# Kernel optimization log

Hardware: AMD Instinct MI355X
Metric: run time of the kernel (lower is better)

The kernel has to match this reference:

```python
import jax, jax.numpy as jnp
import numpy as np

B, C, H, W = 2, 256, 128, 128
L, NH, NP = 4, 8, 4
D = C // NH
HW = H * W


def _pos_emb_2d(h, w, c):
    # positional_encodings.PositionalEncoding2D for channels-last input (B, h, w, c)
    ch = int(np.ceil(c / 4) * 2)
    inv_freq = 1.0 / (10000.0 ** (np.arange(0, ch, 2, dtype=np.float32) / ch))

    def emb(n):
        s = np.arange(n, dtype=np.float32)[:, None] * inv_freq[None, :]
        return np.stack([np.sin(s), np.cos(s)], -1).reshape(n, -1)  # interleaved sin/cos

    out = np.zeros((h, w, 2 * ch), np.float32)
    out[:, :, :ch] = emb(h)[:, None, :]
    out[:, :, ch:2 * ch] = emb(w)[None, :, :]
    return jnp.asarray(out[:, :, :c])


def _offset_bias():
    # init_weights grid_init bias of sampling_offsets
    thetas = np.arange(NH, dtype=np.float32) * (2.0 * np.pi / NH)
    g = np.stack([np.cos(thetas), np.sin(thetas)], -1)
    g = g / np.abs(g).max(-1, keepdims=True)
    g = np.tile(g[:, None, None, :], (1, 1, NP, 1))
    for i in range(NP):
        g[:, :, i, :] *= i + 1
    return np.tile(g.reshape(-1)[None], (L, 1)).astype(np.float32)


def _ref_points(h, w):
    # get_reference_points with scale_ratio == 1 (ratio of equal lidar ranges)
    ry, rx = jnp.meshgrid(jnp.linspace(0.5, h - 0.5, h) / h,
                          jnp.linspace(0.5, w - 0.5, w) / w, indexing='ij')
    return jnp.stack([rx.reshape(-1), ry.reshape(-1)], -1)  # (HW, 2) as (x, y)


def _deform_attn(value, loc, aw, h, w):
    # value: (B,HW,NH,D); loc in [0,1]: (B,HW,NH,NP,2); aw: (B,HW,NH,NP)
    # Matches F.grid_sample(mode='bilinear', padding_mode='zeros', align_corners=False)
    b, q, nh, d = value.shape
    p = loc.shape[3]
    v = value.transpose(0, 2, 1, 3)  # (B, NH, HW, D)
    gx = 2.0 * loc[..., 0] - 1.0
    gy = 2.0 * loc[..., 1] - 1.0
    ix = ((gx + 1.0) * w - 1.0) * 0.5
    iy = ((gy + 1.0) * h - 1.0) * 0.5
    x0 = jnp.floor(ix)
    y0 = jnp.floor(iy)

    def gather(xf, yf):
        valid = (xf >= 0) & (xf <= w - 1) & (yf >= 0) & (yf <= h - 1)
        xi = jnp.clip(xf, 0, w - 1).astype(jnp.int32)
        yi = jnp.clip(yf, 0, h - 1).astype(jnp.int32)
        idx = (yi * w + xi).transpose(0, 2, 1, 3).reshape(b, nh, q * p)
        g = jnp.take_along_axis(v, idx[..., None], axis=2).reshape(b, nh, q, p, d)
        return g * valid.transpose(0, 2, 1, 3)[..., None]

    wx1 = (ix - x0).transpose(0, 2, 1, 3)[..., None]
    wy1 = (iy - y0).transpose(0, 2, 1, 3)[..., None]
    wx0 = 1.0 - wx1
    wy0 = 1.0 - wy1
    s = (gather(x0, y0) * (wx0 * wy0) + gather(x0 + 1.0, y0) * (wx1 * wy0)
         + gather(x0, y0 + 1.0) * (wx0 * wy1) + gather(x0 + 1.0, y0 + 1.0) * (wx1 * wy1))
    out = jnp.einsum('bhqpd,bqhp->bqhd', s, aw)
    return out.reshape(b, q, nh * d)


def setup_inputs() -> dict:
    key = jax.random.key(0)
    ks = jax.random.split(key, 8)
    sc = 1.0 / np.sqrt(C).astype(np.float32)
    return {
        "ego_feature": jax.random.normal(ks[0], (B, C, H, W), jnp.float32),
        "conv_w": jax.random.normal(ks[1], (C, C), jnp.float32) * sc,  # 1x1 conv, (in,out)
        "conv_b": jnp.zeros((C,), jnp.float32),
        "in_scale": jnp.ones((1,), jnp.float32) / 30.0,
        "out_scale": jnp.ones((1,), jnp.float32) / 30.0,
        "off_w": jax.random.normal(ks[2], (L, C, NH * NP * 2), jnp.float32) * 0.01,
        "off_b": jnp.asarray(_offset_bias()),
        "aw_w": jax.random.normal(ks[3], (L, C, NH * NP), jnp.float32) * 0.02,
        "aw_b": jnp.zeros((L, NH * NP), jnp.float32),
        "vp_w": jax.random.normal(ks[4], (L, C, C), jnp.float32) * sc,
        "vp_b": jnp.zeros((L, C), jnp.float32),
        "op_w": jax.random.normal(ks[5], (L, C, C), jnp.float32) * sc,
        "op_b": jnp.zeros((L, C), jnp.float32),
    }


def reference(ego_feature, conv_w, conv_b, in_scale, out_scale, off_w, off_b,
              aw_w, aw_b, vp_w, vp_b, op_w, op_b):
    # PositionalEncodingPermute2D: channels-last PE, permuted to (C,H,W)
    pe_in = _pos_emb_2d(H, W, C).transpose(2, 0, 1)[None]  # (1,C,H,W)
    x = ego_feature + in_scale[0] * pe_in
    key_tok = x.reshape(B, C, HW).transpose(0, 2, 1)  # (B, HW, C)
    # Upsample(scale=1) is identity; 1x1 conv == per-token matmul
    out = key_tok @ conv_w + conv_b
    pe_out = _pos_emb_2d(H, W, C)[None]  # (1,H,W,C)
    ref = _ref_points(H, W)
    norm = jnp.asarray([W, H], jnp.float32)
    for l in range(L):
        o = out.reshape(B, H, W, C) + out_scale[0] * pe_out
        q = o.reshape(B, HW, C)
        identity = q
        v = (key_tok @ vp_w[l] + vp_b[l]).reshape(B, HW, NH, D)
        offs = (q @ off_w[l] + off_b[l]).reshape(B, HW, NH, NP, 2)
        aw = jax.nn.softmax((q @ aw_w[l] + aw_b[l]).reshape(B, HW, NH, NP), axis=-1)
        loc = ref[None, :, None, None, :] + offs / norm
        attn = _deform_attn(v, loc, aw, H, W)
        out = attn @ op_w[l] + op_b[l] + identity  # dropout is identity in eval
    return out  # (B, HW, C)
```

## Files before the change

### kernel.cpp

```cpp
#include <hip/hip_runtime.h>
#include <math.h>

#define HH 128
#define WW 128
#define CCH 256
#define NHH 8
#define NPP 4
#define DDIM 32
#define HWW (HH * WW)
#define BB 2
#define MM (BB * HWW)
#define KK 256

typedef __attribute__((ext_vector_type(8))) __bf16 bf16x8;
typedef __attribute__((ext_vector_type(8))) short s16x8;
typedef __attribute__((ext_vector_type(4))) short s16x4;
typedef __attribute__((ext_vector_type(4))) float f32x4;

#define PE_LOG2_STEP 0.20762050593f

__device__ __forceinline__ float pe_val(int c, int y, int x) {
    int j = (c & 127) >> 1;
    float pos = (c < 128) ? (float)y : (float)x;
    float f = exp2f(-(float)j * PE_LOG2_STEP);
    float s, cs;
    __sincosf(pos * f, &s, &cs);
    return (c & 1) ? cs : s;
}

__device__ __forceinline__ short f2b(float f) {
    union { float f; unsigned u; } c; c.f = f;
    unsigned r = c.u + 0x7FFF + ((c.u >> 16) & 1);
    return (short)(r >> 16);
}

__device__ __forceinline__ float b2f(short s) {
    union { unsigned u; float f; } c;
    c.u = ((unsigned)(unsigned short)s) << 16;
    return c.f;
}

__device__ __forceinline__ void gload16(const short* g, short* l) {
    __builtin_amdgcn_global_load_lds(
        (const __attribute__((address_space(1))) unsigned int*)g,
        (__attribute__((address_space(3))) unsigned int*)l, 16, 0, 0);
}

__global__ __launch_bounds__(256) void pe_table_kernel(
    const float* __restrict__ out_scale, short* __restrict__ pe_b)
{
    int t = blockIdx.x * 256 + threadIdx.x;
    int cp = t & 127;
    int p = t >> 7;
    int y = p >> 7, x = p & 127;
    int c2 = cp * 2;
    int j = (c2 & 127) >> 1;
    float pos = (c2 < 128) ? (float)y : (float)x;
    float f = exp2f(-(float)j * PE_LOG2_STEP);
    float s, c;
    __sincosf(pos * f, &s, &c);
    float sc = out_scale[0];
    pe_b[(size_t)p * CCH + c2] = f2b(sc * s);
    pe_b[(size_t)p * CCH + c2 + 1] = f2b(sc * c);
}

__global__ __launch_bounds__(256) void convert_big_w(
    const float* __restrict__ conv_w, const float* __restrict__ vp_w,
    const float* __restrict__ op_w, short* __restrict__ wt)
{
    __shared__ float tile[32][33];
    int z = blockIdx.z;
    const float* src = (z == 0) ? conv_w
                     : (z <= 4) ? vp_w + (size_t)(z - 1) * KK * CCH
                                : op_w + (size_t)(z - 5) * KK * CCH;
    short* dst = wt + (size_t)z * KK * CCH;
    int k0 = blockIdx.x * 32, n0 = blockIdx.y * 32;
    int tx = threadIdx.x, ty = threadIdx.y;
    #pragma unroll
    for (int i = 0; i < 4; ++i)
        tile[ty + i * 8][tx] = src[(size_t)(k0 + ty + i * 8) * CCH + n0 + tx];
    __syncthreads();
    int t = ty * 32 + tx;
    int n_l = t >> 3, ks = (t & 7) * 4;
    s16x4 o;
    #pragma unroll
    for (int j = 0; j < 4; ++j) o[j] = f2b(tile[ks + j][n_l]);
    *(s16x4*)&dst[(size_t)(n0 + n_l) * KK + k0 + ks] = o;
}

__global__ __launch_bounds__(256) void convert_offaw_w(
    const float* __restrict__ off_w, const float* __restrict__ aw_w,
    const float* __restrict__ off_b, const float* __restrict__ aw_b,
    short* __restrict__ wt, float* __restrict__ bias_cat)
{
    __shared__ float tile[32][33];
    int l = blockIdx.z;
    int nt = blockIdx.y;
    int k0 = blockIdx.x * 32;
    const float* src; int N, ncol0;
    if (nt < 2) { src = off_w + (size_t)l * KK * 64; N = 64; ncol0 = nt * 32; }
    else        { src = aw_w + (size_t)l * KK * 32; N = 32; ncol0 = 0; }
    int tx = threadIdx.x, ty = threadIdx.y;
    #pragma unroll
    for (int i = 0; i < 4; ++i)
        tile[ty + i * 8][tx] = src[(size_t)(k0 + ty + i * 8) * N + ncol0 + tx];
    __syncthreads();
    int t = ty * 32 + tx;
    int n_l = t >> 3, ks = (t & 7) * 4;
    s16x4 o;
    #pragma unroll
    for (int j = 0; j < 4; ++j) o[j] = f2b(tile[ks + j][n_l]);
    *(s16x4*)&wt[((size_t)l * 96 + nt * 32 + n_l) * KK + k0 + ks] = o;
    if (blockIdx.x == 0 && t < 32) {
        int col = nt * 32 + t;
        bias_cat[l * 96 + col] = (nt < 2) ? off_b[l * 64 + ncol0 + t]
                                          : aw_b[l * 32 + t];
    }
}

__global__ __launch_bounds__(256) void transpose_pe_kernel(
    const float* __restrict__ ego, const float* __restrict__ in_scale,
    short* __restrict__ ktb)
{
    __shared__ float tile[32][33];
    int b = blockIdx.z;
    int c0 = blockIdx.x * 32;
    int p0 = blockIdx.y * 32;
    int tx = threadIdx.x, ty = threadIdx.y;
    const float* egob = ego + (size_t)b * CCH * HWW;
    #pragma unroll
    for (int i = 0; i < 4; ++i)
        tile[ty + i * 8][tx] = egob[(size_t)(c0 + ty + i * 8) * HWW + p0 + tx];
    __syncthreads();
    float isc = in_scale[0];
    int t = ty * 32 + tx;
    int p_l = t >> 3, cs = (t & 7) * 4;
    int p = p0 + p_l;
    int y = p >> 7, x = p & 127;
    s16x4 o;
    #pragma unroll
    for (int j = 0; j < 4; ++j) {
        int c = c0 + cs + j;
        o[j] = f2b(tile[cs + j][p_l] + isc * pe_val(c, y, x));
    }
    *(s16x4*)&ktb[((size_t)b * HWW + p) * CCH + c0 + cs] = o;
}

__device__ __forceinline__ void stage_slab64(
    const short* __restrict__ src, short* As, int m0, int w, int lane)
{
    #pragma unroll
    for (int i = 0; i < 8; ++i) {
        int c = w * 64 + i * 256;
        int cc = c + lane;
        int r = cc >> 5, col = cc & 31, ks = col >> 3, u = col & 7;
        gload16(src + (size_t)(m0 + r) * KK + ks * 64 + ((u ^ (r & 7)) << 3),
                As + c * 8);
    }
}

template<int NINST>
__device__ __forceinline__ void stage_tile(
    const short* __restrict__ src, short* dst, int row0, int ks, int w, int lane)
{
    #pragma unroll
    for (int i = 0; i < NINST; ++i) {
        int c = w * 64 + i * 256;
        int cc = c + lane;
        int r = cc >> 3, u = cc & 7;
        gload16(src + (size_t)(row0 + r) * KK + ks * 64 + ((u ^ (r & 7)) << 3),
                dst + c * 8);
    }
}

template<int BM, int BN, int WM, int WN>
__device__ __forceinline__ void gemm_core_db(
    const short* __restrict__ A, const short* __restrict__ Bt,
    short* AsBase, short* BsBase, int m0, int n0, int tid,
    f32x4 (&acc)[WM / 16][WN / 16])
{
    constexpr int MF = WM / 16, NF = WN / 16;
    constexpr int WAVES_N = BN / WN;
    constexpr int A_INST = (BM * 8) / 256;
    constexpr int B_INST = (BN * 8) / 256;
    int w = tid >> 6, lane = tid & 63;
    int g = lane >> 4, l16 = lane & 15;
    int wr = w / WAVES_N, wc = w % WAVES_N;
    short* As0 = AsBase; short* As1 = AsBase + BM * 64;
    short* Bs0 = BsBase; short* Bs1 = BsBase + BN * 64;

    stage_tile<A_INST>(A, As0, m0, 0, w, lane);
    stage_tile<B_INST>(Bt, Bs0, n0, 0, w, lane);
    asm volatile("s_waitcnt vmcnt(0)" ::: "memory");
    __syncthreads();

    #pragma unroll
    for (int ks = 0; ks < 4; ++ks) {
        short* Ac = (ks & 1) ? As1 : As0;
        short* Bc = (ks & 1) ? Bs1 : Bs0;
        short* An = (ks & 1) ? As0 : As1;
        short* Bn = (ks & 1) ? Bs0 : Bs1;
        if (ks < 3) {
            stage_tile<A_INST>(A, An, m0, ks + 1, w, lane);
            stage_tile<B_INST>(Bt, Bn, n0, ks + 1, w, lane);
        }
        #pragma unroll
        for (int kh = 0; kh < 2; ++kh) {
            bf16x8 af[MF], bfr[NF];
            #pragma unroll
            for (int mf = 0; mf < MF; ++mf) {
                int r = wr * WM + mf * 16 + l16, s = kh * 4 + g;
                af[mf] = *(const bf16x8*)(Ac + r * 64 + ((s ^ (r & 7)) * 8));
            }
            #pragma unroll
            for (int nf = 0; nf < NF; ++nf) {
                int r = wc * WN + nf * 16 + l16, s = kh * 4 + g;
                bfr[nf] = *(const bf16x8*)(Bc + r * 64 + ((s ^ (r & 7)) * 8));
            }
            #pragma unroll
            for (int mf = 0; mf < MF; ++mf)
                #pragma unroll
                for (int nf = 0; nf < NF; ++nf)
                    acc[mf][nf] = __builtin_amdgcn_mfma_f32_16x16x32_bf16(
                        af[mf], bfr[nf], acc[mf][nf], 0, 0, 0);
        }
        if (ks < 3) {
            __builtin_amdgcn_sched_barrier(0);
            asm volatile("s_waitcnt vmcnt(0)" ::: "memory");
            __syncthreads();
        }
    }
}

__global__ __launch_bounds__(256) void gemm_conv_v(
    const short* __restrict__ ktb, const short* __restrict__ wt_big,
    const float* __restrict__ conv_b, const float* __restrict__ vp_b,
    const short* __restrict__ pe_b, short* __restrict__ qb,
    short* __restrict__ vb16)
{
    __shared__ short As[64 * 256];
    __shared__ short Bs[2 * 128 * 64];
    int tid = threadIdx.x;
    int w = tid >> 6, lane = tid & 63;
    int g = lane >> 4, l16 = lane & 15;
    int wr = w >> 1, wc = w & 1;
    int flat = blockIdx.x;
    int xcd = flat & 7;
    int idx = flat >> 3;
    int mloc = idx & 63;
    int n0 = (idx >> 6) * 128;
    int m0 = (xcd * 64 + mloc) * 64;

    stage_slab64(ktb, As, m0, w, lane);
    s16x8 rb[4];
    #pragma unroll
    for (int i = 0; i < 4; ++i) {
        int task = tid + i * 256; int r = task >> 3, s = task & 7;
        rb[i] = *(const s16x8*)(wt_big + (size_t)(n0 + r) * KK + s * 8);
    }
    asm volatile("s_waitcnt vmcnt(0)" ::: "memory");
    __syncthreads();

    for (int z = 0; z < 5; ++z) {
        f32x4 acc[2][4] = {};
        for (int ks = 0; ks < 4; ++ks) {
            int t = z * 4 + ks;
            short* Bcur = Bs + (t & 1) * (128 * 64);
            #pragma unroll
            for (int i = 0; i < 4; ++i) {
                int task = tid + i * 256; int r = task >> 3, s = task & 7;
                *(s16x8*)&Bcur[r * 64 + ((s ^ (r & 7)) * 8)] = rb[i];
            }
            __syncthreads();
            if (t < 19) {
                int tn = t + 1;
                const short* Bz = wt_big + (size_t)(tn >> 2) * KK * CCH + (tn & 3) * 64;
                #pragma unroll
                for (int i = 0; i < 4; ++i) {
                    int task = tid + i * 256; int r = task >> 3, s = task & 7;
                    rb[i] = *(const s16x8*)(Bz + (size_t)(n0 + r) * KK + s * 8);
                }
            }
            #pragma unroll
            for (int kh = 0; kh < 2; ++kh) {
                int s = kh * 4 + g;
                bf16x8 af[2], bfr[4];
                #pragma unroll
                for (int mf = 0; mf < 2; ++mf) {
                    int r = wr * 32 + mf * 16 + l16;
                    af[mf] = *(const bf16x8*)(As + r * 256 + (ks * 8 + (s ^ (r & 7))) * 8);
                }
                #pragma unroll
                for (int nf = 0; nf < 4; ++nf) {
                    int r = wc * 64 + nf * 16 + l16;
                    bfr[nf] = *(const bf16x8*)(Bcur + r * 64 + ((s ^ (r & 7)) * 8));
                }
                #pragma unroll
                for (int mf = 0; mf < 2; ++mf)
                    #pragma unroll
                    for (int nf = 0; nf < 4; ++nf)
                        acc[mf][nf] = __builtin_amdgcn_mfma_f32_16x16x32_bf16(
                            af[mf], bfr[nf], acc[mf][nf], 0, 0, 0);
            }
        }
        const float* bias = (z == 0) ? conv_b : vp_b + (size_t)(z - 1) * CCH;
        short* vz = vb16 + (size_t)(z - 1) * MM * CCH;
        #pragma unroll
        for (int mf = 0; mf < 2; ++mf) {
            #pragma unroll
            for (int nf = 0; nf < 4; ++nf) {
                int col = n0 + wc * 64 + nf * 16 + l16;
                float bv = bias[col];
                #pragma unroll
                for (int j = 0; j < 4; ++j) {
                    int row = m0 + wr * 32 + mf * 16 + g * 4 + j;
                    float vv = acc[mf][nf][j] + bv;
                    if (z == 0) {
                        int p = row & (HWW - 1);
                        qb[(size_t)row * CCH + col] =
                            f2b(vv + b2f(pe_b[(size_t)p * CCH + col]));
                    } else {
                        int b = row >> 14, p = row & (HWW - 1);
                        int h = col >> 5, d = col & 31;
                        vz[(((size_t)(b * NHH + h)) * HWW + p) * DDIM + d] = f2b(vv);
                    }
                }
            }
        }
    }
}

__global__ __launch_bounds__(256) void gemm_scores(
    const short* __restrict__ qb, const short* __restrict__ wt,
    const float* __restrict__ bias, float* __restrict__ scores)
{
    __shared__ short As[2 * 64 * 64];
    __shared__ short Bs[2 * 96 * 64];
    int tid = threadIdx.x;
    int m0 = blockIdx.y * 64;
    f32x4 acc[2][3] = {};
    gemm_core_db<64, 96, 32, 48>(qb, wt, As, Bs, m0, 0, tid, acc);

    int w = tid >> 6, lane = tid & 63;
    int g = lane >> 4, l16 = lane & 15;
    int wr = w >> 1, wc = w & 1;
    #pragma unroll
    for (int mf = 0; mf < 2; ++mf) {
        #pragma unroll
        for (int nf = 0; nf < 3; ++nf) {
            int col = wc * 48 + nf * 16 + l16;
            float bv = bias[col];
            #pragma unroll
            for (int j = 0; j < 4; ++j) {
                int row = m0 + wr * 32 + mf * 16 + g * 4 + j;
                scores[(size_t)row * 96 + col] = acc[mf][nf][j] + bv;
            }
        }
    }
}

template<bool FINAL>
__global__ __launch_bounds__(256) void gemm_op(
    const short* __restrict__ attnb, const short* __restrict__ wt,
    const float* __restrict__ bias, const short* __restrict__ pe_b,
    float* __restrict__ outf, short* __restrict__ qb)
{
    __shared__ short As[2 * 128 * 64];
    __shared__ short Bs[2 * 128 * 64];
    int tid = threadIdx.x;
    int flat = blockIdx.x;
    int xcd = flat & 7;
    int idx = flat >> 3;
    int mloc = idx & 31;
    int n0 = (idx >> 5) * 128;
    int m0 = (xcd * 32 + mloc) * 128;
    f32x4 acc[4][4] = {};
    gemm_core_db<128, 128, 64, 64>(attnb, wt, As, Bs, m0, n0, tid, acc);

    int w = tid >> 6, lane = tid & 63;
    int g = lane >> 4, l16 = lane & 15;
    int wr = w >> 1, wc = w & 1;
    #pragma unroll
    for (int mf = 0; mf < 4; ++mf) {
        #pragma unroll
        for (int nf = 0; nf < 4; ++nf) {
            int col = n0 + wc * 64 + nf * 16 + l16;
            float bv = bias[col];
            #pragma unroll
            for (int j = 0; j < 4; ++j) {
                int row = m0 + wr * 64 + mf * 16 + g * 4 + j;
                float vv = acc[mf][nf][j] + bv + b2f(qb[(size_t)row * CCH + col]);
                if (FINAL) {
                    outf[(size_t)row * CCH + col] = vv;
                } else {
                    int p = row & (HWW - 1);
                    qb[(size_t)row * CCH + col] =
                        f2b(vv + b2f(pe_b[(size_t)p * CCH + col]));
                }
            }
        }
    }
}

__device__ __forceinline__ void fma8(uint4 u, float w, float* a) {
    a[0] = fmaf(__uint_as_float(u.x << 16), w, a[0]);
    a[1] = fmaf(__uint_as_float(u.x & 0xffff0000u), w, a[1]);
    a[2] = fmaf(__uint_as_float(u.y << 16), w, a[2]);
    a[3] = fmaf(__uint_as_float(u.y & 0xffff0000u), w, a[3]);
    a[4] = fmaf(__uint_as_float(u.z << 16), w, a[4]);
    a[5] = fmaf(__uint_as_float(u.z & 0xffff0000u), w, a[5]);
    a[6] = fmaf(__uint_as_float(u.w << 16), w, a[6]);
    a[7] = fmaf(__uint_as_float(u.w & 0xffff0000u), w, a[7]);
}

__global__ __launch_bounds__(256) void deform_kernel(
    const short* __restrict__ vb16, const float* __restrict__ scores,
    short* __restrict__ attnb)
{
    int tid = threadIdx.x;
    int gi = tid >> 2;
    int dl = (tid & 3) * 8;
    int flat = blockIdx.x;
    int xcd = flat & 7;
    int idx = flat >> 3;
    int bh = xcd * 2 + (idx >> 8);
    int tile = idx & 255;
    int b = bh >> 3, h = bh & 7;
    int y = (tile >> 4) * 8 + (gi >> 3);
    int x = (tile & 15) * 8 + (gi & 7);
    int p = (y << 7) + x;
    long bp = (long)b * HWW + p;
    const float* srow = scores + bp * 96;
    float4 sc4 = *(const float4*)(srow + 64 + h * 4);
    float mx = fmaxf(fmaxf(sc4.x, sc4.y), fmaxf(sc4.z, sc4.w));
    float e0 = __expf(sc4.x - mx), e1 = __expf(sc4.y - mx);
    float e2 = __expf(sc4.z - mx), e3 = __expf(sc4.w - mx);
    float inv = 1.f / (e0 + e1 + e2 + e3);
    float wa4[4] = {e0 * inv, e1 * inv, e2 * inv, e3 * inv};
    float4 o01 = *(const float4*)(srow + h * 8);
    float4 o23 = *(const float4*)(srow + h * 8 + 4);
    float oxs[4] = {o01.x, o01.z, o23.x, o23.z};
    float oys[4] = {o01.y, o01.w, o23.y, o23.w};
    const short* vbase = vb16 + ((size_t)bh * HWW) * DDIM + dl;
    float a[8] = {};
    #pragma unroll
    for (int pt = 0; pt < NPP; ++pt) {
        float wa = wa4[pt];
        float ix = (float)x + oxs[pt];
        float iy = (float)y + oys[pt];
        float x0f = floorf(ix), y0f = floorf(iy);
        float fx = ix - x0f, fy = iy - y0f;
        float wx0 = (x0f >= 0.f && x0f <= 127.f) ? (1.f - fx) : 0.f;
        float wx1 = (x0f >= -1.f && x0f <= 126.f) ? fx : 0.f;
        float wy0 = ((y0f >= 0.f && y0f <= 127.f) ? (1.f - fy) : 0.f) * wa;
        float wy1 = ((y0f >= -1.f && y0f <= 126.f) ? fy : 0.f) * wa;
        int xi0 = (int)fminf(fmaxf(x0f, 0.f), 127.f);
        int yi0 = (int)fminf(fmaxf(y0f, 0.f), 127.f);
        int xi1 = (int)fminf(fmaxf(x0f + 1.f, 0.f), 127.f);
        int yi1 = (int)fminf(fmaxf(y0f + 1.f, 0.f), 127.f);
        int r0 = yi0 << 7, r1 = yi1 << 7;
        uint4 u00 = *(const uint4*)(vbase + (size_t)(r0 + xi0) * DDIM);
        uint4 u01 = *(const uint4*)(vbase + (size_t)(r0 + xi1) * DDIM);
        uint4 u10 = *(const uint4*)(vbase + (size_t)(r1 + xi0) * DDIM);
        uint4 u11 = *(const uint4*)(vbase + (size_t)(r1 + xi1) * DDIM);
        fma8(u00, wx0 * wy0, a);
        fma8(u01, wx1 * wy0, a);
        fma8(u10, wx0 * wy1, a);
        fma8(u11, wx1 * wy1, a);
    }
    s16x8 o;
    #pragma unroll
    for (int j = 0; j < 8; ++j) o[j] = f2b(a[j]);
    *(s16x8*)&attnb[bp * CCH + h * DDIM + dl] = o;
}

extern "C" void kernel_launch(void* const* d_in, const int* in_sizes, int n_in,
                              void* d_out, int out_size, void* d_ws, size_t ws_size,
                              hipStream_t stream) {
    const float* ego       = (const float*)d_in[0];
    const float* conv_w    = (const float*)d_in[1];
    const float* conv_b    = (const float*)d_in[2];
    const float* in_scale  = (const float*)d_in[3];
    const float* out_scale = (const float*)d_in[4];
    const float* off_w     = (const float*)d_in[5];
    const float* off_b     = (const float*)d_in[6];
    const float* aw_w      = (const float*)d_in[7];
    const float* aw_b      = (const float*)d_in[8];
    const float* vp_w      = (const float*)d_in[9];
    const float* vp_b      = (const float*)d_in[10];
    const float* op_w      = (const float*)d_in[11];
    const float* op_b      = (const float*)d_in[12];
    float* out = (float*)d_out;

    float* scores   = (float*)d_ws;
    float* bias_cat = scores + (size_t)MM * 96;
    short* pe_b     = (short*)(bias_cat + 4 * 96);
    short* ktb      = pe_b + (size_t)HWW * CCH;
    short* qb       = ktb + (size_t)MM * CCH;
    short* vb16     = qb + (size_t)MM * CCH;
    short* attnb    = vb16 + (size_t)4 * MM * CCH;
    short* wt_big   = attnb + (size_t)MM * CCH;
    short* wt_offaw = wt_big + (size_t)9 * KK * CCH;

    pe_table_kernel<<<HWW * 128 / 256, 256, 0, stream>>>(out_scale, pe_b);
    convert_big_w<<<dim3(8, 8, 9), dim3(32, 8), 0, stream>>>(conv_w, vp_w, op_w, wt_big);
    convert_offaw_w<<<dim3(8, 3, 4), dim3(32, 8), 0, stream>>>(
        off_w, aw_w, off_b, aw_b, wt_offaw, bias_cat);
    transpose_pe_kernel<<<dim3(8, 512, 2), dim3(32, 8), 0, stream>>>(ego, in_scale, ktb);

    gemm_conv_v<<<1024, 256, 0, stream>>>(
        ktb, wt_big, conv_b, vp_b, pe_b, qb, vb16);

    for (int l = 0; l < 4; ++l) {
        gemm_scores<<<dim3(1, 512), 256, 0, stream>>>(
            qb, wt_offaw + (size_t)l * 96 * KK, bias_cat + l * 96, scores);
        deform_kernel<<<4096, 256, 0, stream>>>(
            vb16 + (size_t)l * MM * CCH, scores, attnb);
        if (l < 3) {
            gemm_op<false><<<512, 256, 0, stream>>>(
                attnb, wt_big + (size_t)(5 + l) * KK * CCH, op_b + l * CCH,
                pe_b, nullptr, qb);
        } else {
            gemm_op<true><<<512, 256, 0, stream>>>(
                attnb, wt_big + (size_t)(5 + l) * KK * CCH, op_b + l * CCH,
                pe_b, out, qb);
        }
    }
}
```

Baseline: 224.6 us.

## Split bilinear corner loads across lane pairs and single-buffer weight tiles in conv GEMM

The deform kernel now uses 8 threads per (query, head) instead of 4. Each half of the group loads the left or right x-corner, which halves the gathers per thread, and the two halves are summed with a lane shuffle before one of them writes the output. The x index clamp is widened to -1 so adjacent columns come from one offset. The query-to-block mapping drops the XCD-aware spatial tiling in favour of a linear order. Separately, the conv/V GEMM moves from a double-buffered to a single-buffered B tile with an extra barrier, cutting LDS use at the cost of more synchronisation.

```diff
diff --git a/kernel.cpp b/kernel.cpp
--- a/kernel.cpp
+++ b/kernel.cpp
@@ -239,7 +239,7 @@
     short* __restrict__ vb16)
 {
     __shared__ short As[64 * 256];
-    __shared__ short Bs[2 * 128 * 64];
+    __shared__ short Bs[128 * 64];
     int tid = threadIdx.x;
     int w = tid >> 6, lane = tid & 63;
     int g = lane >> 4, l16 = lane & 15;
@@ -264,17 +264,22 @@
     for (int z = 0; z < 5; ++z) {
         f32x4 acc[2][4] = {};
         for (int ks = 0; ks < 4; ++ks) {
-            int t = z * 4 + ks;
-            short* Bcur = Bs + (t & 1) * (128 * 64);
+            __syncthreads();
             #pragma unroll
             for (int i = 0; i < 4; ++i) {
                 int task = tid + i * 256; int r = task >> 3, s = task & 7;
-                *(s16x8*)&Bcur[r * 64 + ((s ^ (r & 7)) * 8)] = rb[i];
+                *(s16x8*)&Bs[r * 64 + ((s ^ (r & 7)) * 8)] = rb[i];
             }
             __syncthreads();
-            if (t < 19) {
-                int tn = t + 1;
-                const short* Bz = wt_big + (size_t)(tn >> 2) * KK * CCH + (tn & 3) * 64;
+            if (ks < 3) {
+                const short* Bz = wt_big + (size_t)z * KK * CCH;
+                #pragma unroll
+                for (int i = 0; i < 4; ++i) {
+                    int task = tid + i * 256; int r = task >> 3, s = task & 7;
+                    rb[i] = *(const s16x8*)(Bz + (size_t)(n0 + r) * KK + (ks + 1) * 64 + s * 8);
+                }
+            } else if (z < 4) {
+                const short* Bz = wt_big + (size_t)(z + 1) * KK * CCH;
                 #pragma unroll
                 for (int i = 0; i < 4; ++i) {
                     int task = tid + i * 256; int r = task >> 3, s = task & 7;
@@ -293,7 +298,7 @@
                 #pragma unroll
                 for (int nf = 0; nf < 4; ++nf) {
                     int r = wc * 64 + nf * 16 + l16;
-                    bfr[nf] = *(const bf16x8*)(Bcur + r * 64 + ((s ^ (r & 7)) * 8));
+                    bfr[nf] = *(const bf16x8*)(Bs + r * 64 + ((s ^ (r & 7)) * 8));
                 }
                 #pragma unroll
                 for (int mf = 0; mf < 2; ++mf)
@@ -418,18 +423,16 @@
     short* __restrict__ attnb)
 {
     int tid = threadIdx.x;
-    int gi = tid >> 2;
-    int dl = (tid & 3) * 8;
-    int flat = blockIdx.x;
-    int xcd = flat & 7;
-    int idx = flat >> 3;
-    int bh = xcd * 2 + (idx >> 8);
-    int tile = idx & 255;
-    int b = bh >> 3, h = bh & 7;
-    int y = (tile >> 4) * 8 + (gi >> 3);
-    int x = (tile & 15) * 8 + (gi & 7);
-    int p = (y << 7) + x;
-    long bp = (long)b * HWW + p;
+    int gi = tid >> 3;
+    int lane8 = tid & 7;
+    int xside = lane8 >> 2;
+    int dl = (lane8 & 3) * 8;
+    long gid = (long)blockIdx.x * 32 + gi;
+    int h = (int)(gid & 7);
+    long bp = gid >> 3;
+    int p = (int)(bp & (HWW - 1));
+    int b = (int)(bp >> 14);
+    int y = p >> 7, x = p & 127;
     const float* srow = scores + bp * 96;
     float4 sc4 = *(const float4*)(srow + 64 + h * 4);
     float mx = fmaxf(fmaxf(sc4.x, sc4.y), fmaxf(sc4.z, sc4.w));
@@ -441,7 +444,7 @@
     float4 o23 = *(const float4*)(srow + h * 8 + 4);
     float oxs[4] = {o01.x, o01.z, o23.x, o23.z};
     float oys[4] = {o01.y, o01.w, o23.y, o23.w};
-    const short* vbase = vb16 + ((size_t)bh * HWW) * DDIM + dl;
+    const short* vbase = vb16 + (size_t)(b * NHH + h) * HWW * DDIM;
     float a[8] = {};
     #pragma unroll
     for (int pt = 0; pt < NPP; ++pt) {
@@ -450,28 +453,29 @@
         float iy = (float)y + oys[pt];
         float x0f = floorf(ix), y0f = floorf(iy);
         float fx = ix - x0f, fy = iy - y0f;
-        float wx0 = (x0f >= 0.f && x0f <= 127.f) ? (1.f - fx) : 0.f;
-        float wx1 = (x0f >= -1.f && x0f <= 126.f) ? fx : 0.f;
+        float wx0v = (x0f >= 0.f && x0f <= 127.f) ? (1.f - fx) : 0.f;
+        float wx1v = (x0f >= -1.f && x0f <= 126.f) ? fx : 0.f;
+        float wxl = xside ? wx1v : wx0v;
         float wy0 = ((y0f >= 0.f && y0f <= 127.f) ? (1.f - fy) : 0.f) * wa;
         float wy1 = ((y0f >= -1.f && y0f <= 126.f) ? fy : 0.f) * wa;
-        int xi0 = (int)fminf(fmaxf(x0f, 0.f), 127.f);
+        int xs = (int)fminf(fmaxf(x0f, -1.f), 127.f);
         int yi0 = (int)fminf(fmaxf(y0f, 0.f), 127.f);
-        int xi1 = (int)fminf(fmaxf(x0f + 1.f, 0.f), 127.f);
         int yi1 = (int)fminf(fmaxf(y0f + 1.f, 0.f), 127.f);
-        int r0 = yi0 << 7, r1 = yi1 << 7;
-        uint4 u00 = *(const uint4*)(vbase + (size_t)(r0 + xi0) * DDIM);
-        uint4 u01 = *(const uint4*)(vbase + (size_t)(r0 + xi1) * DDIM);
-        uint4 u10 = *(const uint4*)(vbase + (size_t)(r1 + xi0) * DDIM);
-        uint4 u11 = *(const uint4*)(vbase + (size_t)(r1 + xi1) * DDIM);
-        fma8(u00, wx0 * wy0, a);
-        fma8(u01, wx1 * wy0, a);
-        fma8(u10, wx0 * wy1, a);
-        fma8(u11, wx1 * wy1, a);
-    }
-    s16x8 o;
-    #pragma unroll
-    for (int j = 0; j < 8; ++j) o[j] = f2b(a[j]);
-    *(s16x8*)&attnb[bp * CCH + h * DDIM + dl] = o;
+        long off0 = (long)(yi0 * WW + xs) * DDIM + xside * DDIM + dl;
+        long off1 = (long)(yi1 * WW + xs) * DDIM + xside * DDIM + dl;
+        uint4 u0 = *(const uint4*)(vbase + off0);
+        uint4 u1 = *(const uint4*)(vbase + off1);
+        fma8(u0, wxl * wy0, a);
+        fma8(u1, wxl * wy1, a);
+    }
+    #pragma unroll
+    for (int j = 0; j < 8; ++j) a[j] += __shfl_xor(a[j], 4);
+    if (xside == 0) {
+        s16x8 o;
+        #pragma unroll
+        for (int j = 0; j < 8; ++j) o[j] = f2b(a[j]);
+        *(s16x8*)&attnb[bp * CCH + h * DDIM + dl] = o;
+    }
 }
 
 extern "C" void kernel_launch(void* const* d_in, const int* in_sizes, int n_in,
@@ -514,7 +518,7 @@
     for (int l = 0; l < 4; ++l) {
         gemm_scores<<<dim3(1, 512), 256, 0, stream>>>(
             qb, wt_offaw + (size_t)l * 96 * KK, bias_cat + l * 96, scores);
-        deform_kernel<<<4096, 256, 0, stream>>>(
+        deform_kernel<<<MM * NHH / 32, 256, 0, stream>>>(
             vb16 + (size_t)l * MM * CCH, scores, attnb);
         if (l < 3) {
             gemm_op<false><<<512, 256, 0, stream>>>(
```

Result: slower. 231.6 us (+3.1%).
